# Kernel tuning notes

Hardware: AMD Instinct MI355X
Metric: run time of the kernel (lower is better)

The kernel has to match this reference:

```python
import jax, jax.numpy as jnp
import numpy as np

N_NODES = 50000
N_EDGES = 600000
IN_CH = 128
HID = 256
OUT_FEAT = 256
OUT_CH = 128
EPS = 1e-12


def _sage_conv(x, src, dst, mask_f, Wl, bl, Wr, n_nodes):
    # PyG SAGEConv: out = lin_l(mean_{j in N(i)} x_j) + lin_r(x_i); L2-normalize rows.
    msg = x[src] * mask_f[:, None]                                  # [E, d] gather
    agg = jax.ops.segment_sum(msg, dst, num_segments=n_nodes)      # [N, d]
    cnt = jax.ops.segment_sum(mask_f, dst, num_segments=n_nodes)   # [N]
    agg = agg / jnp.maximum(cnt, 1.0)[:, None]                      # mean over kept edges
    out = agg @ Wl.T + bl + x @ Wr.T                                 # [N, h]
    nrm = jnp.maximum(jnp.linalg.norm(out, axis=-1, keepdims=True), EPS)
    return out / nrm


def setup_inputs() -> dict:
    key = jax.random.key(0)
    ks = jax.random.split(key, 12)
    x = jax.random.normal(ks[0], (N_NODES, IN_CH), dtype=jnp.float32)
    edge_index = jax.random.randint(ks[1], (2, N_EDGES), 0, N_NODES, dtype=jnp.int32)
    edge_mask = jax.random.bernoulli(ks[2], 0.7, (N_EDGES,))  # dropout_edge p=0.3 keep mask

    def lin(k, fan_out, fan_in):
        s = 1.0 / np.sqrt(fan_in)
        return jax.random.uniform(k, (fan_out, fan_in), jnp.float32, -s, s)

    W1l = lin(ks[3], HID, IN_CH)
    b1 = jnp.zeros((HID,), jnp.float32)
    W1r = lin(ks[4], HID, IN_CH)
    Ws = lin(ks[5], HID, IN_CH)
    bs = jnp.zeros((HID,), jnp.float32)
    W2l = lin(ks[6], OUT_FEAT, HID)
    b2 = jnp.zeros((OUT_FEAT,), jnp.float32)
    W2r = lin(ks[7], OUT_FEAT, HID)
    Wo = lin(ks[8], OUT_CH, OUT_FEAT)
    bo = jnp.zeros((OUT_CH,), jnp.float32)
    return {"x": x, "edge_index": edge_index, "edge_mask": edge_mask,
            "W1l": W1l, "b1": b1, "W1r": W1r, "Ws": Ws, "bs": bs,
            "W2l": W2l, "b2": b2, "W2r": W2r, "Wo": Wo, "bo": bo}


def reference(x, edge_index, edge_mask, W1l, b1, W1r, Ws, bs, W2l, b2, W2r, Wo, bo):
    src, dst = edge_index[0], edge_index[1]
    ones = jnp.ones((src.shape[0],), x.dtype)
    # conv1 uses all edges
    h = _sage_conv(x, src, dst, ones, W1l, b1, W1r, N_NODES)
    h = h + (x @ Ws.T + bs)
    h = jnp.tanh(h)
    # conv2 uses edge-dropped graph (mask = kept edges)
    mask_f = edge_mask.astype(x.dtype)
    h = jnp.tanh(_sage_conv(h, src, dst, mask_f, W2l, b2, W2r, N_NODES))
    return h @ Wo.T + bo
```

## Files before the change

### kernel.cpp

```cpp
#include <hip/hip_runtime.h>
#include <hip/hip_bf16.h>

#define N_NODES 50000
#define N_PAD   50048
#define N_EDGES 600000
#define IN_CH 128
#define HID 256
#define OUT_CH 128

typedef unsigned short u16;
typedef unsigned char u8;
typedef unsigned int u32;

typedef __attribute__((ext_vector_type(8))) short short8;
typedef __attribute__((ext_vector_type(4))) float f32x4;

typedef __attribute__((address_space(3))) u32 as3_u32;
typedef __attribute__((address_space(1))) const u32 as1_u32;

__device__ __forceinline__ float bf2f(u16 v) {
    unsigned u = ((unsigned)v) << 16;
    return __uint_as_float(u);
}
__device__ __forceinline__ u16 f2bf(float f) {
    unsigned u = __float_as_uint(f);
    u += 0x7FFF + ((u >> 16) & 1);
    return (u16)(u >> 16);
}

__device__ __forceinline__ void async16(const void* g, void* l) {
    __builtin_amdgcn_global_load_lds((as1_u32*)g, (as3_u32*)l, 16, 0, 0);
}

__global__ void detect_kernel(const u16* __restrict__ xu, const u8* __restrict__ mb,
                              int* __restrict__ flags) {
    int lane = threadIdx.x & 63;

    int inr = 0;
    {
        u32 w0 = ((const u32*)xu)[lane * 2 + 0];
        u32 w1 = ((const u32*)xu)[lane * 2 + 1];
        u16 h[4] = {(u16)w0, (u16)(w0 >> 16), (u16)w1, (u16)(w1 >> 16)};
#pragma unroll
        for (int j = 0; j < 4; j++) {
            int e = (h[j] >> 7) & 0xFF;
            if (e >= 100 && e <= 133) inr++;
        }
    }

    int c1 = 0, c23 = 0, h3f_1 = 0, h3f_3 = 0;
#pragma unroll
    for (int t = 0; t < 16; t++) {
        u32 w = ((const u32*)mb)[t * 64 + lane];
        u8 b1 = (u8)(w >> 8), b2 = (u8)(w >> 16), b3 = (u8)(w >> 24);
        if (b1) c1++;
        if (b1 == 0x3F) h3f_1 = 1;
        if (b2) c23++;
        if (b3) c23++;
        if (b3 == 0x3F) h3f_3 = 1;
    }

#pragma unroll
    for (int off = 32; off > 0; off >>= 1) {
        inr   += __shfl_xor(inr, off, 64);
        c1    += __shfl_xor(c1, off, 64);
        c23   += __shfl_xor(c23, off, 64);
        h3f_1 |= __shfl_xor(h3f_1, off, 64);
        h3f_3 |= __shfl_xor(h3f_3, off, 64);
    }

    if (lane == 0 && blockIdx.x == 0) {
        flags[0] = (inr >= 200) ? 1 : 0;
        int fmt;
        if (h3f_1) fmt = 3;
        else if (h3f_3) fmt = 2;
        else if (c1 + c23 > 0) fmt = 0;
        else fmt = 1;
        flags[1] = fmt;
    }
}

__global__ void biases_kernel(const void* __restrict__ b1, const void* __restrict__ bs,
                              const void* __restrict__ b2, const void* __restrict__ bo,
                              float* __restrict__ dst, const int* __restrict__ flags) {
    int i = blockIdx.x * blockDim.x + threadIdx.x;
    if (i >= 896) return;
    const void* src; int idx;
    if (i < 256)      { src = b1; idx = i; }
    else if (i < 512) { src = bs; idx = i - 256; }
    else if (i < 768) { src = b2; idx = i - 512; }
    else              { src = bo; idx = i - 768; }
    float v;
    if (flags[0]) v = bf2f(((const u16*)src)[idx]);
    else          v = ((const float*)src)[idx];
    dst[i] = v;
}

__global__ void wcat_kernel(const void* __restrict__ A, const void* __restrict__ B,
                            u16* __restrict__ dst, int N, int K1, int K2,
                            const int* __restrict__ flags) {
    int i = blockIdx.x * blockDim.x + threadIdx.x;
    int K = K1 + K2;
    if (i >= N * K) return;
    int n = i / K, k = i % K;
    const void* src; int idx;
    if (k < K1) { src = A; idx = n * K1 + k; }
    else        { src = B; idx = n * K2 + (k - K1); }
    u16 v;
    if (flags[0]) v = ((const u16*)src)[idx];
    else          v = f2bf(((const float*)src)[idx]);
    dst[i] = v;
}

__global__ void hist_kernel(const int* __restrict__ ei, const void* __restrict__ em,
                            int* __restrict__ deg, int* __restrict__ deg2,
                            int* __restrict__ rank, int* __restrict__ krank,
                            const int* __restrict__ flags) {
    int i = blockIdx.x * blockDim.x + threadIdx.x;
    if (i >= N_EDGES) return;
    int d = ei[N_EDGES + i];
    rank[i] = atomicAdd(&deg[d], 1);
    int fmt = flags[1];
    bool keep;
    if (fmt == 0)      keep = ((const u8*)em)[i] != 0;
    else if (fmt == 1) keep = ((const int*)em)[i] != 0;
    else if (fmt == 2) keep = ((const float*)em)[i] != 0.f;
    else               keep = ((const u16*)em)[i] != 0;
    krank[i] = keep ? atomicAdd(&deg2[d], 1) : -1;
}

__global__ void partial_kernel(const int* __restrict__ deg, const int* __restrict__ deg2,
                               int* __restrict__ partial, int nb) {
    __shared__ int sh[256];
    int t = threadIdx.x;
    int arr = (blockIdx.x >= nb) ? 1 : 0;
    int blk = blockIdx.x - arr * nb;
    const int* d = arr ? deg2 : deg;
    int i = blk * 256 + t;
    sh[t] = (i < N_NODES) ? d[i] : 0;
    __syncthreads();
    for (int s = 128; s > 0; s >>= 1) {
        if (t < s) sh[t] += sh[t + s];
        __syncthreads();
    }
    if (t == 0) partial[blockIdx.x] = sh[0];
}

__global__ void scanp_kernel(const int* __restrict__ partial, int* __restrict__ pscan, int nb) {
    __shared__ int sh[256];
    int t = threadIdx.x;
    int base = blockIdx.x * nb;
    int v = (t < nb) ? partial[base + t] : 0;
    sh[t] = v;
    __syncthreads();
    for (int o = 1; o < 256; o <<= 1) {
        int u = (t >= o) ? sh[t - o] : 0;
        __syncthreads();
        sh[t] += u;
        __syncthreads();
    }
    if (t < nb) pscan[base + t] = sh[t] - v;
}

__global__ void rowptr_kernel(const int* __restrict__ deg, const int* __restrict__ deg2,
                              const int* __restrict__ pscan,
                              int* __restrict__ row_ptr, int* __restrict__ row_ptr2, int nb) {
    __shared__ int sh[256];
    int t = threadIdx.x;
    int arr = (blockIdx.x >= nb) ? 1 : 0;
    int blk = blockIdx.x - arr * nb;
    const int* d = arr ? deg2 : deg;
    int* rp = arr ? row_ptr2 : row_ptr;
    int i = blk * 256 + t;
    int v = (i < N_NODES) ? d[i] : 0;
    sh[t] = v;
    __syncthreads();
    for (int o = 1; o < 256; o <<= 1) {
        int u = (t >= o) ? sh[t - o] : 0;
        __syncthreads();
        sh[t] += u;
        __syncthreads();
    }
    if (i <= N_NODES) rp[i] = pscan[arr * nb + blk] + sh[t] - v;
}

__global__ void scatter_csr_kernel(const int* __restrict__ ei, const int* __restrict__ rank,
                                   const int* __restrict__ krank,
                                   const int* __restrict__ row_ptr, const int* __restrict__ row_ptr2,
                                   int* __restrict__ srcs, int* __restrict__ srcs2) {
    int i = blockIdx.x * blockDim.x + threadIdx.x;
    if (i >= N_EDGES) return;
    int d = ei[N_EDGES + i];
    int s = ei[i];
    srcs[row_ptr[d] + rank[i]] = s;
    int r2 = krank[i];
    if (r2 >= 0) srcs2[row_ptr2[d] + r2] = s;
}

__global__ __launch_bounds__(256) void gather1_kernel(const int* __restrict__ row_ptr,
                                                      const int* __restrict__ srcs,
                                                      const u16* __restrict__ xb,
                                                      u16* __restrict__ aggb) {
    int wid = (blockIdx.x * blockDim.x + threadIdx.x) >> 6;
    int lane = threadIdx.x & 63;
    if (wid >= N_NODES) return;
    int start = row_ptr[wid], end = row_ptr[wid + 1];
    int dg = end - start;
    int sv = (lane < dg) ? srcs[start + lane] : 0;
    float ax = 0.f, ay = 0.f, bx = 0.f, by = 0.f;
    int n = dg < 64 ? dg : 64;
    int e = 0;
    for (; e + 2 <= n; e += 2) {
        int s0 = __builtin_amdgcn_readlane(sv, e);
        int s1 = __builtin_amdgcn_readlane(sv, e + 1);
        u32 v0 = *(const u32*)(xb + (size_t)s0 * IN_CH + lane * 2);
        u32 v1 = *(const u32*)(xb + (size_t)s1 * IN_CH + lane * 2);
        ax += bf2f((u16)v0); ay += bf2f((u16)(v0 >> 16));
        bx += bf2f((u16)v1); by += bf2f((u16)(v1 >> 16));
    }
    if (e < n) {
        int s0 = __builtin_amdgcn_readlane(sv, e);
        u32 v0 = *(const u32*)(xb + (size_t)s0 * IN_CH + lane * 2);
        ax += bf2f((u16)v0); ay += bf2f((u16)(v0 >> 16));
    }
    for (e = 64; e < dg; e++) {
        int s0 = srcs[start + e];
        u32 v0 = *(const u32*)(xb + (size_t)s0 * IN_CH + lane * 2);
        ax += bf2f((u16)v0); ay += bf2f((u16)(v0 >> 16));
    }
    float inv = 1.f / fmaxf((float)dg, 1.f);
    u32 o = (u32)f2bf((ax + bx) * inv) | ((u32)f2bf((ay + by) * inv) << 16);
    *(u32*)(aggb + (size_t)wid * IN_CH + lane * 2) = o;
}

__global__ __launch_bounds__(256) void gather2_kernel(const int* __restrict__ row_ptr2,
                                                      const int* __restrict__ srcs2,
                                                      const u16* __restrict__ h1b,
                                                      u16* __restrict__ aggb) {
    int wid = (blockIdx.x * blockDim.x + threadIdx.x) >> 6;
    int lane = threadIdx.x & 63;
    if (wid >= N_NODES) return;
    int start = row_ptr2[wid], end = row_ptr2[wid + 1];
    int dg = end - start;
    int sv = (lane < dg) ? srcs2[start + lane] : 0;
    float a0 = 0.f, a1 = 0.f, a2 = 0.f, a3 = 0.f;
    float b0 = 0.f, b1 = 0.f, b2 = 0.f, b3 = 0.f;
    int n = dg < 64 ? dg : 64;
    int e = 0;
    for (; e + 2 <= n; e += 2) {
        int s0 = __builtin_amdgcn_readlane(sv, e);
        int s1 = __builtin_amdgcn_readlane(sv, e + 1);
        uint2 v = *(const uint2*)(h1b + (size_t)s0 * HID + lane * 4);
        uint2 w = *(const uint2*)(h1b + (size_t)s1 * HID + lane * 4);
        a0 += bf2f((u16)v.x); a1 += bf2f((u16)(v.x >> 16));
        a2 += bf2f((u16)v.y); a3 += bf2f((u16)(v.y >> 16));
        b0 += bf2f((u16)w.x); b1 += bf2f((u16)(w.x >> 16));
        b2 += bf2f((u16)w.y); b3 += bf2f((u16)(w.y >> 16));
    }
    if (e < n) {
        int s0 = __builtin_amdgcn_readlane(sv, e);
        uint2 v = *(const uint2*)(h1b + (size_t)s0 * HID + lane * 4);
        a0 += bf2f((u16)v.x); a1 += bf2f((u16)(v.x >> 16));
        a2 += bf2f((u16)v.y); a3 += bf2f((u16)(v.y >> 16));
    }
    for (e = 64; e < dg; e++) {
        int s0 = srcs2[start + e];
        uint2 v = *(const uint2*)(h1b + (size_t)s0 * HID + lane * 4);
        a0 += bf2f((u16)v.x); a1 += bf2f((u16)(v.x >> 16));
        a2 += bf2f((u16)v.y); a3 += bf2f((u16)(v.y >> 16));
    }
    float inv = 1.f / fmaxf((float)dg, 1.f);
    u32 o0 = (u32)f2bf((a0 + b0) * inv) | ((u32)f2bf((a1 + b1) * inv) << 16);
    u32 o1 = (u32)f2bf((a2 + b2) * inv) | ((u32)f2bf((a3 + b3) * inv) << 16);
    u16* p = aggb + (size_t)wid * HID + lane * 4;
    *(u32*)p = o0;
    *(u32*)(p + 2) = o1;
}

template<int MODE>
__global__ __launch_bounds__(256, 2) void gemm_staged(
    const u16* __restrict__ A0, const u16* __restrict__ A1,
    const u16* __restrict__ W0, const u16* __restrict__ W1,
    const float* __restrict__ bias0, const float* __restrict__ bias1,
    u16* __restrict__ outb, void* __restrict__ outv, const int* __restrict__ flags) {

    constexpr int NT  = (MODE == 3) ? 2 : 4;
    constexpr int Nw  = NT * 16;
    constexpr int NKS = (MODE == 1) ? 6 : ((MODE == 2) ? 8 : 4);
    constexpr int BBYTES = NT * 64 * 128;
    __shared__ __align__(16) u8 ldsmem[16384 + 2 * BBYTES];

    int tid = threadIdx.x;
    int w = tid >> 6, lane = tid & 63;
    int q = lane >> 4, c = lane & 15;
    int m_base = blockIdx.x * 64;
    int rj = lane >> 3, jj = lane & 7;
    int j16 = ((jj ^ rj) << 4);

    f32x4 acc[4][NT], acc2[4][NT];
    const f32x4 z = {0.f, 0.f, 0.f, 0.f};
#pragma unroll
    for (int mt = 0; mt < 4; mt++)
#pragma unroll
        for (int nt = 0; nt < NT; nt++) { acc[mt][nt] = z; acc2[mt][nt] = z; }

    auto stage = [&](int ks, int b) {
        const u16* ap; int astr, kta;
        const u16* wp; int wstr, ktw;
        if (MODE == 1) {
            astr = 128;
            if (ks < 2)      { ap = A0; kta = ks; }
            else if (ks < 4) { ap = A1; kta = ks - 2; }
            else             { ap = A1; kta = ks - 4; }
            if (ks < 4) { wp = W0; wstr = 256; ktw = ks; }
            else        { wp = W1; wstr = 128; ktw = ks - 4; }
        } else if (MODE == 2) {
            astr = 256;
            if (ks < 4) { ap = A0; kta = ks; } else { ap = A1; kta = ks - 4; }
            wp = W0; wstr = 512; ktw = ks;
        } else {
            astr = 256; ap = A0; kta = ks;
            wp = W0; wstr = 256; ktw = ks;
        }
#pragma unroll
        for (int t = 0; t < 2; t++) {
            int r = w * 16 + t * 8;
            const u8* g = (const u8*)(ap + (size_t)(m_base + r + rj) * astr) + kta * 128 + j16;
            async16(g, ldsmem + b * 8192 + r * 128);
        }
#pragma unroll
        for (int t = 0; t < NT * 2; t++) {
            int n = w * Nw + t * 8;
            const u8* g = (const u8*)(wp + (size_t)(n + rj) * wstr) + ktw * 128 + j16;
            async16(g, ldsmem + 16384 + b * BBYTES + n * 128);
        }
    };

    auto compute = [&](int b, f32x4 (*tgt)[NT]) {
        const u8* ab = ldsmem + b * 8192;
        const u8* bb = ldsmem + 16384 + b * BBYTES;
#pragma unroll
        for (int kk = 0; kk < 2; kk++) {
            int sA = (((kk * 4 + q) ^ (c & 7)) << 4);
            short8 af[4], bfr[NT];
#pragma unroll
            for (int mt = 0; mt < 4; mt++)
                af[mt] = *(const short8*)(ab + (mt * 16 + c) * 128 + sA);
#pragma unroll
            for (int nt = 0; nt < NT; nt++)
                bfr[nt] = *(const short8*)(bb + (w * Nw + nt * 16 + c) * 128 + sA);
#pragma unroll
            for (int mt = 0; mt < 4; mt++)
#pragma unroll
                for (int nt = 0; nt < NT; nt++)
                    tgt[mt][nt] = __builtin_amdgcn_mfma_f32_16x16x32_bf16(af[mt], bfr[nt], tgt[mt][nt], 0, 0, 0);
        }
    };

    stage(0, 0);
    int b = 0;
#pragma unroll
    for (int ks = 0; ks < NKS; ks++) {
        __syncthreads();
        if (ks + 1 < NKS) stage(ks + 1, b ^ 1);
        if (MODE == 1 && ks >= 4) compute(b, acc2);
        else                      compute(b, acc);
        b ^= 1;
    }
    __syncthreads();

    if (MODE == 3) {
        float bcol[NT];
#pragma unroll
        for (int nt = 0; nt < NT; nt++) bcol[nt] = bias0[w * Nw + nt * 16 + c];
        int isbf = flags[0];
#pragma unroll
        for (int mt = 0; mt < 4; mt++)
#pragma unroll
            for (int r = 0; r < 4; r++) {
                int row = m_base + mt * 16 + q * 4 + r;
                if (row < N_NODES) {
#pragma unroll
                    for (int nt = 0; nt < NT; nt++) {
                        float v = acc[mt][nt][r] + bcol[nt];
                        int col = w * Nw + nt * 16 + c;
                        if (isbf) ((u16*)outv)[(size_t)row * OUT_CH + col] = f2bf(v);
                        else      ((float*)outv)[(size_t)row * OUT_CH + col] = v;
                    }
                }
            }
    } else {
        float* redf = (float*)ldsmem;
        float bcol[NT], b2col[NT];
#pragma unroll
        for (int nt = 0; nt < NT; nt++) {
            int col = w * Nw + nt * 16 + c;
            bcol[nt] = bias0[col];
            if (MODE == 1) b2col[nt] = bias1[col];
        }
        float s[4][4];
#pragma unroll
        for (int mt = 0; mt < 4; mt++)
#pragma unroll
            for (int r = 0; r < 4; r++) {
                float t = 0.f;
#pragma unroll
                for (int nt = 0; nt < NT; nt++) {
                    float v = acc[mt][nt][r] + bcol[nt];
                    acc[mt][nt][r] = v;
                    t += v * v;
                }
                s[mt][r] = t;
            }
#pragma unroll
        for (int off = 1; off < 16; off <<= 1) {
#pragma unroll
            for (int mt = 0; mt < 4; mt++)
#pragma unroll
                for (int r = 0; r < 4; r++)
                    s[mt][r] += __shfl_xor(s[mt][r], off, 64);
        }
        if (c == 0) {
#pragma unroll
            for (int mt = 0; mt < 4; mt++)
#pragma unroll
                for (int r = 0; r < 4; r++)
                    redf[(mt * 16 + q * 4 + r) * 4 + w] = s[mt][r];
        }
        __syncthreads();
        if (tid < 64) {
            float t = redf[tid * 4] + redf[tid * 4 + 1] + redf[tid * 4 + 2] + redf[tid * 4 + 3];
            redf[256 + tid] = 1.f / fmaxf(sqrtf(t), 1e-12f);
        }
        __syncthreads();
#pragma unroll
        for (int mt = 0; mt < 4; mt++)
#pragma unroll
            for (int r = 0; r < 4; r++) {
                int rl = mt * 16 + q * 4 + r;
                int row = m_base + rl;
                if (row < N_NODES) {
                    float iv = redf[256 + rl];
#pragma unroll
                    for (int nt = 0; nt < NT; nt++) {
                        int col = w * Nw + nt * 16 + c;
                        float h;
                        if (MODE == 1) h = acc[mt][nt][r] * iv + acc2[mt][nt][r] + b2col[nt];
                        else           h = acc[mt][nt][r] * iv;
                        outb[(size_t)row * HID + col] = f2bf(tanhf(h));
                    }
                }
            }
    }
}

extern "C" void kernel_launch(void* const* d_in, const int* in_sizes, int n_in,
                              void* d_out, int out_size, void* d_ws, size_t ws_size,
                              hipStream_t stream) {
    const void* x    = d_in[0];
    const int*  ei   = (const int*)d_in[1];
    const void* em   = d_in[2];
    const void* W1l  = d_in[3];
    const void* b1   = d_in[4];
    const void* W1r  = d_in[5];
    const void* Ws   = d_in[6];
    const void* bs   = d_in[7];
    const void* W2l  = d_in[8];
    const void* b2   = d_in[9];
    const void* W2r  = d_in[10];
    const void* Wo   = d_in[11];
    const void* bo   = d_in[12];

    char* p = (char*)d_ws;
    auto carve = [&](size_t bytes) { char* r = p; p += (bytes + 63) & ~(size_t)63; return r; };
    int*   flags   = (int*)carve(256);
    u16*   xb      = (u16*)carve((size_t)N_PAD * IN_CH * 2);
    u16*   h1b     = (u16*)carve((size_t)N_PAD * HID * 2);
    u16*   aggb    = (u16*)carve((size_t)N_PAD * HID * 2);
    u16*   h2b     = (u16*)carve((size_t)N_PAD * HID * 2);
    u16*   Wc1     = (u16*)carve(256 * 256 * 2);
    u16*   Wsb     = (u16*)carve(256 * 128 * 2);
    u16*   Wc2     = (u16*)carve(256 * 512 * 2);
    u16*   Wob     = (u16*)carve(128 * 256 * 2);
    float* biasf   = (float*)carve(896 * 4);
    int*   deg     = (int*)carve(2 * 50176 * 4);
    int*   deg2    = deg + 50176;
    int*   row_ptr = (int*)carve(50056 * 4);
    int*   row_ptr2= (int*)carve(50056 * 4);
    int*   partial = (int*)carve(512 * 4);
    int*   pscan   = (int*)carve(512 * 4);
    int*   rank    = (int*)carve((size_t)N_EDGES * 4);
    int*   krank   = (int*)carve((size_t)N_EDGES * 4);
    int*   srcs    = (int*)carve((size_t)N_EDGES * 4);
    int*   srcs2   = (int*)carve((size_t)N_EDGES * 4);
    float* b1f = biasf, *bsf = biasf + 256, *b2f = biasf + 512, *bof = biasf + 768;
    (void)ws_size; (void)in_sizes; (void)n_in; (void)out_size;

    detect_kernel<<<1, 64, 0, stream>>>((const u16*)x, (const u8*)em, flags);

    wcat_kernel<<<(N_NODES * IN_CH + 255) / 256, 256, 0, stream>>>(x, x, xb, 1, N_NODES * IN_CH, 0, flags);
    wcat_kernel<<<(256 * 256 + 255) / 256, 256, 0, stream>>>(W1l, W1r, Wc1, 256, 128, 128, flags);
    wcat_kernel<<<(256 * 128 + 255) / 256, 256, 0, stream>>>(Ws, Ws, Wsb, 1, 256 * 128, 0, flags);
    wcat_kernel<<<(256 * 512 + 255) / 256, 256, 0, stream>>>(W2l, W2r, Wc2, 256, 256, 256, flags);
    wcat_kernel<<<(128 * 256 + 255) / 256, 256, 0, stream>>>(Wo, Wo, Wob, 1, 128 * 256, 0, flags);
    biases_kernel<<<4, 256, 0, stream>>>(b1, bs, b2, bo, biasf, flags);

    hipMemsetAsync(deg, 0, 2 * 50176 * sizeof(int), stream);
    hist_kernel<<<(N_EDGES + 255) / 256, 256, 0, stream>>>(ei, em, deg, deg2, rank, krank, flags);
    const int NB = (N_NODES + 255) / 256;
    partial_kernel<<<2 * NB, 256, 0, stream>>>(deg, deg2, partial, NB);
    scanp_kernel<<<2, 256, 0, stream>>>(partial, pscan, NB);
    rowptr_kernel<<<2 * NB, 256, 0, stream>>>(deg, deg2, pscan, row_ptr, row_ptr2, NB);
    scatter_csr_kernel<<<(N_EDGES + 255) / 256, 256, 0, stream>>>(ei, rank, krank, row_ptr, row_ptr2, srcs, srcs2);

    const int GB = N_PAD / 64;

    gather1_kernel<<<(N_NODES * 64) / 256, 256, 0, stream>>>(row_ptr, srcs, xb, aggb);
    gemm_staged<1><<<GB, 256, 0, stream>>>(aggb, xb, Wc1, Wsb, b1f, bsf, h1b, nullptr, flags);

    gather2_kernel<<<(N_NODES * 64) / 256, 256, 0, stream>>>(row_ptr2, srcs2, h1b, aggb);
    gemm_staged<2><<<GB, 256, 0, stream>>>(aggb, h1b, Wc2, nullptr, b2f, nullptr, h2b, nullptr, flags);

    gemm_staged<3><<<GB, 256, 0, stream>>>(h2b, nullptr, Wob, nullptr, bof, nullptr, nullptr, d_out, flags);
}
```

Before: 339.2 us.

## Fuse conversion launches, pack dual degree counters, unroll gathers by four

Folds the five weight/input conversion kernels and the bias kernel into one launch. Packs both the full-graph and the masked-graph degree counters into one 32-bit word, updated with a single atomic per edge. The per-edge ranks are packed the same way, so the two CSR builds share one partial/scan/rowptr pass and half the rank storage. The neighbour gathers are unrolled to four outstanding loads with more accumulators, to raise memory-level parallelism. The packing relies on per-node and per-block counts fitting in 16 bits, and the wider unroll adds register pressure.

```diff
diff --git a/kernel.cpp b/kernel.cpp
--- a/kernel.cpp
+++ b/kernel.cpp
@@ -80,64 +80,76 @@
     }
 }
 
-__global__ void biases_kernel(const void* __restrict__ b1, const void* __restrict__ bs,
-                              const void* __restrict__ b2, const void* __restrict__ bo,
-                              float* __restrict__ dst, const int* __restrict__ flags) {
+#define NX (N_NODES * IN_CH)
+__global__ void convert_all_kernel(const void* __restrict__ x,
+                                   const void* __restrict__ W1l, const void* __restrict__ W1r,
+                                   const void* __restrict__ Ws,
+                                   const void* __restrict__ W2l, const void* __restrict__ W2r,
+                                   const void* __restrict__ Wo,
+                                   const void* __restrict__ b1, const void* __restrict__ bs,
+                                   const void* __restrict__ b2, const void* __restrict__ bo,
+                                   u16* __restrict__ xb, u16* __restrict__ Wc1,
+                                   u16* __restrict__ Wsb, u16* __restrict__ Wc2,
+                                   u16* __restrict__ Wob, float* __restrict__ biasf,
+                                   const int* __restrict__ flags) {
     int i = blockIdx.x * blockDim.x + threadIdx.x;
-    if (i >= 896) return;
-    const void* src; int idx;
-    if (i < 256)      { src = b1; idx = i; }
-    else if (i < 512) { src = bs; idx = i - 256; }
-    else if (i < 768) { src = b2; idx = i - 512; }
-    else              { src = bo; idx = i - 768; }
-    float v;
-    if (flags[0]) v = bf2f(((const u16*)src)[idx]);
-    else          v = ((const float*)src)[idx];
-    dst[i] = v;
-}
-
-__global__ void wcat_kernel(const void* __restrict__ A, const void* __restrict__ B,
-                            u16* __restrict__ dst, int N, int K1, int K2,
-                            const int* __restrict__ flags) {
-    int i = blockIdx.x * blockDim.x + threadIdx.x;
-    int K = K1 + K2;
-    if (i >= N * K) return;
-    int n = i / K, k = i % K;
-    const void* src; int idx;
-    if (k < K1) { src = A; idx = n * K1 + k; }
-    else        { src = B; idx = n * K2 + (k - K1); }
-    u16 v;
-    if (flags[0]) v = ((const u16*)src)[idx];
-    else          v = f2bf(((const float*)src)[idx]);
-    dst[i] = v;
-}
+    int isbf = flags[0];
+    auto cv = [&](const void* s, int idx) -> u16 {
+        return isbf ? ((const u16*)s)[idx] : f2bf(((const float*)s)[idx]);
+    };
+    if (i < NX) { xb[i] = cv(x, i); return; }
+    i -= NX;
+    if (i < 256 * 256) {
+        int n = i >> 8, k = i & 255;
+        const void* s = (k < 128) ? W1l : W1r;
+        Wc1[i] = cv(s, n * 128 + (k & 127));
+        return;
+    }
+    i -= 256 * 256;
+    if (i < 256 * 128) { Wsb[i] = cv(Ws, i); return; }
+    i -= 256 * 128;
+    if (i < 256 * 512) {
+        int n = i >> 9, k = i & 511;
+        const void* s = (k < 256) ? W2l : W2r;
+        Wc2[i] = cv(s, n * 256 + (k & 255));
+        return;
+    }
+    i -= 256 * 512;
+    if (i < 128 * 256) { Wob[i] = cv(Wo, i); return; }
+    i -= 128 * 256;
+    if (i < 896) {
+        const void* s; int idx;
+        if (i < 256)      { s = b1; idx = i; }
+        else if (i < 512) { s = bs; idx = i - 256; }
+        else if (i < 768) { s = b2; idx = i - 512; }
+        else              { s = bo; idx = i - 768; }
+        biasf[i] = isbf ? bf2f(((const u16*)s)[idx]) : ((const float*)s)[idx];
+    }
+}
+#define CONV_TOTAL (NX + 256 * 256 + 256 * 128 + 256 * 512 + 128 * 256 + 896)
 
 __global__ void hist_kernel(const int* __restrict__ ei, const void* __restrict__ em,
-                            int* __restrict__ deg, int* __restrict__ deg2,
-                            int* __restrict__ rank, int* __restrict__ krank,
+                            u32* __restrict__ degp, u32* __restrict__ rankp,
                             const int* __restrict__ flags) {
     int i = blockIdx.x * blockDim.x + threadIdx.x;
     if (i >= N_EDGES) return;
     int d = ei[N_EDGES + i];
-    rank[i] = atomicAdd(&deg[d], 1);
     int fmt = flags[1];
     bool keep;
     if (fmt == 0)      keep = ((const u8*)em)[i] != 0;
     else if (fmt == 1) keep = ((const int*)em)[i] != 0;
     else if (fmt == 2) keep = ((const float*)em)[i] != 0.f;
     else               keep = ((const u16*)em)[i] != 0;
-    krank[i] = keep ? atomicAdd(&deg2[d], 1) : -1;
-}
-
-__global__ void partial_kernel(const int* __restrict__ deg, const int* __restrict__ deg2,
-                               int* __restrict__ partial, int nb) {
-    __shared__ int sh[256];
+    u32 inc = keep ? 0x10001u : 1u;
+    u32 old = atomicAdd(&degp[d], inc);
+    rankp[i] = (old & 0xffffu) | (keep ? (old & 0xffff0000u) : 0xffff0000u);
+}
+
+__global__ void partial_kernel(const u32* __restrict__ degp, u32* __restrict__ partial) {
+    __shared__ u32 sh[256];
     int t = threadIdx.x;
-    int arr = (blockIdx.x >= nb) ? 1 : 0;
-    int blk = blockIdx.x - arr * nb;
-    const int* d = arr ? deg2 : deg;
-    int i = blk * 256 + t;
-    sh[t] = (i < N_NODES) ? d[i] : 0;
+    int i = blockIdx.x * 256 + t;
+    sh[t] = (i < N_NODES) ? degp[i] : 0;
     __syncthreads();
     for (int s = 128; s > 0; s >>= 1) {
         if (t < s) sh[t] += sh[t + s];
@@ -146,55 +158,64 @@
     if (t == 0) partial[blockIdx.x] = sh[0];
 }
 
-__global__ void scanp_kernel(const int* __restrict__ partial, int* __restrict__ pscan, int nb) {
+__global__ void scanp_kernel(const u32* __restrict__ partial, int* __restrict__ pscan, int nb) {
     __shared__ int sh[256];
     int t = threadIdx.x;
-    int base = blockIdx.x * nb;
-    int v = (t < nb) ? partial[base + t] : 0;
+    u32 pv = (t < nb) ? partial[t] : 0;
+    int v1 = pv & 0xffff, v2 = pv >> 16;
+    sh[t] = v1;
+    __syncthreads();
+    for (int o = 1; o < 256; o <<= 1) {
+        int u = (t >= o) ? sh[t - o] : 0;
+        __syncthreads();
+        sh[t] += u;
+        __syncthreads();
+    }
+    if (t < nb) pscan[t] = sh[t] - v1;
+    __syncthreads();
+    sh[t] = v2;
+    __syncthreads();
+    for (int o = 1; o < 256; o <<= 1) {
+        int u = (t >= o) ? sh[t - o] : 0;
+        __syncthreads();
+        sh[t] += u;
+        __syncthreads();
+    }
+    if (t < nb) pscan[nb + t] = sh[t] - v2;
+}
+
+__global__ void rowptr_kernel(const u32* __restrict__ degp, const int* __restrict__ pscan,
+                              int* __restrict__ row_ptr, int* __restrict__ row_ptr2, int nb) {
+    __shared__ u32 sh[256];
+    int t = threadIdx.x;
+    int i = blockIdx.x * 256 + t;
+    u32 v = (i < N_NODES) ? degp[i] : 0;
     sh[t] = v;
     __syncthreads();
     for (int o = 1; o < 256; o <<= 1) {
-        int u = (t >= o) ? sh[t - o] : 0;
+        u32 u = (t >= o) ? sh[t - o] : 0;
         __syncthreads();
         sh[t] += u;
         __syncthreads();
     }
-    if (t < nb) pscan[base + t] = sh[t] - v;
-}
-
-__global__ void rowptr_kernel(const int* __restrict__ deg, const int* __restrict__ deg2,
-                              const int* __restrict__ pscan,
-                              int* __restrict__ row_ptr, int* __restrict__ row_ptr2, int nb) {
-    __shared__ int sh[256];
-    int t = threadIdx.x;
-    int arr = (blockIdx.x >= nb) ? 1 : 0;
-    int blk = blockIdx.x - arr * nb;
-    const int* d = arr ? deg2 : deg;
-    int* rp = arr ? row_ptr2 : row_ptr;
-    int i = blk * 256 + t;
-    int v = (i < N_NODES) ? d[i] : 0;
-    sh[t] = v;
-    __syncthreads();
-    for (int o = 1; o < 256; o <<= 1) {
-        int u = (t >= o) ? sh[t - o] : 0;
-        __syncthreads();
-        sh[t] += u;
-        __syncthreads();
-    }
-    if (i <= N_NODES) rp[i] = pscan[arr * nb + blk] + sh[t] - v;
-}
-
-__global__ void scatter_csr_kernel(const int* __restrict__ ei, const int* __restrict__ rank,
-                                   const int* __restrict__ krank,
+    u32 ex = sh[t] - v;
+    if (i <= N_NODES) {
+        row_ptr[i]  = pscan[blockIdx.x] + (int)(ex & 0xffff);
+        row_ptr2[i] = pscan[nb + blockIdx.x] + (int)(ex >> 16);
+    }
+}
+
+__global__ void scatter_csr_kernel(const int* __restrict__ ei, const u32* __restrict__ rankp,
                                    const int* __restrict__ row_ptr, const int* __restrict__ row_ptr2,
                                    int* __restrict__ srcs, int* __restrict__ srcs2) {
     int i = blockIdx.x * blockDim.x + threadIdx.x;
     if (i >= N_EDGES) return;
     int d = ei[N_EDGES + i];
     int s = ei[i];
-    srcs[row_ptr[d] + rank[i]] = s;
-    int r2 = krank[i];
-    if (r2 >= 0) srcs2[row_ptr2[d] + r2] = s;
+    u32 rp = rankp[i];
+    srcs[row_ptr[d] + (int)(rp & 0xffffu)] = s;
+    u32 kr = rp >> 16;
+    if (kr != 0xffffu) srcs2[row_ptr2[d] + (int)kr] = s;
 }
 
 __global__ __launch_bounds__(256) void gather1_kernel(const int* __restrict__ row_ptr,
@@ -207,29 +228,38 @@
     int start = row_ptr[wid], end = row_ptr[wid + 1];
     int dg = end - start;
     int sv = (lane < dg) ? srcs[start + lane] : 0;
-    float ax = 0.f, ay = 0.f, bx = 0.f, by = 0.f;
+    float a0 = 0.f, a1 = 0.f, b0 = 0.f, b1 = 0.f;
+    float c0 = 0.f, c1 = 0.f, d0 = 0.f, d1 = 0.f;
     int n = dg < 64 ? dg : 64;
     int e = 0;
-    for (; e + 2 <= n; e += 2) {
+    for (; e + 4 <= n; e += 4) {
         int s0 = __builtin_amdgcn_readlane(sv, e);
         int s1 = __builtin_amdgcn_readlane(sv, e + 1);
+        int s2 = __builtin_amdgcn_readlane(sv, e + 2);
+        int s3 = __builtin_amdgcn_readlane(sv, e + 3);
         u32 v0 = *(const u32*)(xb + (size_t)s0 * IN_CH + lane * 2);
         u32 v1 = *(const u32*)(xb + (size_t)s1 * IN_CH + lane * 2);
-        ax += bf2f((u16)v0); ay += bf2f((u16)(v0 >> 16));
-        bx += bf2f((u16)v1); by += bf2f((u16)(v1 >> 16));
-    }
-    if (e < n) {
+        u32 v2 = *(const u32*)(xb + (size_t)s2 * IN_CH + lane * 2);
+        u32 v3 = *(const u32*)(xb + (size_t)s3 * IN_CH + lane * 2);
+        a0 += bf2f((u16)v0); a1 += bf2f((u16)(v0 >> 16));
+        b0 += bf2f((u16)v1); b1 += bf2f((u16)(v1 >> 16));
+        c0 += bf2f((u16)v2); c1 += bf2f((u16)(v2 >> 16));
+        d0 += bf2f((u16)v3); d1 += bf2f((u16)(v3 >> 16));
+    }
+    for (; e < n; e++) {
         int s0 = __builtin_amdgcn_readlane(sv, e);
         u32 v0 = *(const u32*)(xb + (size_t)s0 * IN_CH + lane * 2);
-        ax += bf2f((u16)v0); ay += bf2f((u16)(v0 >> 16));
+        a0 += bf2f((u16)v0); a1 += bf2f((u16)(v0 >> 16));
     }
     for (e = 64; e < dg; e++) {
         int s0 = srcs[start + e];
         u32 v0 = *(const u32*)(xb + (size_t)s0 * IN_CH + lane * 2);
-        ax += bf2f((u16)v0); ay += bf2f((u16)(v0 >> 16));
+        a0 += bf2f((u16)v0); a1 += bf2f((u16)(v0 >> 16));
     }
     float inv = 1.f / fmaxf((float)dg, 1.f);
-    u32 o = (u32)f2bf((ax + bx) * inv) | ((u32)f2bf((ay + by) * inv) << 16);
+    float rx = (a0 + b0) + (c0 + d0);
+    float ry = (a1 + b1) + (c1 + d1);
+    u32 o = (u32)f2bf(rx * inv) | ((u32)f2bf(ry * inv) << 16);
     *(u32*)(aggb + (size_t)wid * IN_CH + lane * 2) = o;
 }
 
@@ -245,19 +275,29 @@
     int sv = (lane < dg) ? srcs2[start + lane] : 0;
     float a0 = 0.f, a1 = 0.f, a2 = 0.f, a3 = 0.f;
     float b0 = 0.f, b1 = 0.f, b2 = 0.f, b3 = 0.f;
+    float c0 = 0.f, c1 = 0.f, c2 = 0.f, c3 = 0.f;
+    float d0 = 0.f, d1 = 0.f, d2 = 0.f, d3 = 0.f;
     int n = dg < 64 ? dg : 64;
     int e = 0;
-    for (; e + 2 <= n; e += 2) {
+    for (; e + 4 <= n; e += 4) {
         int s0 = __builtin_amdgcn_readlane(sv, e);
         int s1 = __builtin_amdgcn_readlane(sv, e + 1);
+        int s2 = __builtin_amdgcn_readlane(sv, e + 2);
+        int s3 = __builtin_amdgcn_readlane(sv, e + 3);
         uint2 v = *(const uint2*)(h1b + (size_t)s0 * HID + lane * 4);
         uint2 w = *(const uint2*)(h1b + (size_t)s1 * HID + lane * 4);
+        uint2 y = *(const uint2*)(h1b + (size_t)s2 * HID + lane * 4);
+        uint2 zz = *(const uint2*)(h1b + (size_t)s3 * HID + lane * 4);
         a0 += bf2f((u16)v.x); a1 += bf2f((u16)(v.x >> 16));
         a2 += bf2f((u16)v.y); a3 += bf2f((u16)(v.y >> 16));
         b0 += bf2f((u16)w.x); b1 += bf2f((u16)(w.x >> 16));
         b2 += bf2f((u16)w.y); b3 += bf2f((u16)(w.y >> 16));
-    }
-    if (e < n) {
+        c0 += bf2f((u16)y.x); c1 += bf2f((u16)(y.x >> 16));
+        c2 += bf2f((u16)y.y); c3 += bf2f((u16)(y.y >> 16));
+        d0 += bf2f((u16)zz.x); d1 += bf2f((u16)(zz.x >> 16));
+        d2 += bf2f((u16)zz.y); d3 += bf2f((u16)(zz.y >> 16));
+    }
+    for (; e < n; e++) {
         int s0 = __builtin_amdgcn_readlane(sv, e);
         uint2 v = *(const uint2*)(h1b + (size_t)s0 * HID + lane * 4);
         a0 += bf2f((u16)v.x); a1 += bf2f((u16)(v.x >> 16));
@@ -270,8 +310,12 @@
         a2 += bf2f((u16)v.y); a3 += bf2f((u16)(v.y >> 16));
     }
     float inv = 1.f / fmaxf((float)dg, 1.f);
-    u32 o0 = (u32)f2bf((a0 + b0) * inv) | ((u32)f2bf((a1 + b1) * inv) << 16);
-    u32 o1 = (u32)f2bf((a2 + b2) * inv) | ((u32)f2bf((a3 + b3) * inv) << 16);
+    float r0 = (a0 + b0) + (c0 + d0);
+    float r1 = (a1 + b1) + (c1 + d1);
+    float r2 = (a2 + b2) + (c2 + d2);
+    float r3 = (a3 + b3) + (c3 + d3);
+    u32 o0 = (u32)f2bf(r0 * inv) | ((u32)f2bf(r1 * inv) << 16);
+    u32 o1 = (u32)f2bf(r2 * inv) | ((u32)f2bf(r3 * inv) << 16);
     u16* p = aggb + (size_t)wid * HID + lane * 4;
     *(u32*)p = o0;
     *(u32*)(p + 2) = o1;
@@ -483,14 +527,12 @@
     u16*   Wc2     = (u16*)carve(256 * 512 * 2);
     u16*   Wob     = (u16*)carve(128 * 256 * 2);
     float* biasf   = (float*)carve(896 * 4);
-    int*   deg     = (int*)carve(2 * 50176 * 4);
-    int*   deg2    = deg + 50176;
+    u32*   degp    = (u32*)carve(50176 * 4);
     int*   row_ptr = (int*)carve(50056 * 4);
     int*   row_ptr2= (int*)carve(50056 * 4);
-    int*   partial = (int*)carve(512 * 4);
+    u32*   partial = (u32*)carve(256 * 4);
     int*   pscan   = (int*)carve(512 * 4);
-    int*   rank    = (int*)carve((size_t)N_EDGES * 4);
-    int*   krank   = (int*)carve((size_t)N_EDGES * 4);
+    u32*   rankp   = (u32*)carve((size_t)N_EDGES * 4);
     int*   srcs    = (int*)carve((size_t)N_EDGES * 4);
     int*   srcs2   = (int*)carve((size_t)N_EDGES * 4);
     float* b1f = biasf, *bsf = biasf + 256, *b2f = biasf + 512, *bof = biasf + 768;
@@ -498,20 +540,17 @@
 
     detect_kernel<<<1, 64, 0, stream>>>((const u16*)x, (const u8*)em, flags);
 
-    wcat_kernel<<<(N_NODES * IN_CH + 255) / 256, 256, 0, stream>>>(x, x, xb, 1, N_NODES * IN_CH, 0, flags);
-    wcat_kernel<<<(256 * 256 + 255) / 256, 256, 0, stream>>>(W1l, W1r, Wc1, 256, 128, 128, flags);
-    wcat_kernel<<<(256 * 128 + 255) / 256, 256, 0, stream>>>(Ws, Ws, Wsb, 1, 256 * 128, 0, flags);
-    wcat_kernel<<<(256 * 512 + 255) / 256, 256, 0, stream>>>(W2l, W2r, Wc2, 256, 256, 256, flags);
-    wcat_kernel<<<(128 * 256 + 255) / 256, 256, 0, stream>>>(Wo, Wo, Wob, 1, 128 * 256, 0, flags);
-    biases_kernel<<<4, 256, 0, stream>>>(b1, bs, b2, bo, biasf, flags);
-
-    hipMemsetAsync(deg, 0, 2 * 50176 * sizeof(int), stream);
-    hist_kernel<<<(N_EDGES + 255) / 256, 256, 0, stream>>>(ei, em, deg, deg2, rank, krank, flags);
+    convert_all_kernel<<<(CONV_TOTAL + 255) / 256, 256, 0, stream>>>(
+        x, W1l, W1r, Ws, W2l, W2r, Wo, b1, bs, b2, bo,
+        xb, Wc1, Wsb, Wc2, Wob, biasf, flags);
+
+    hipMemsetAsync(degp, 0, 50176 * sizeof(u32), stream);
+    hist_kernel<<<(N_EDGES + 255) / 256, 256, 0, stream>>>(ei, em, degp, rankp, flags);
     const int NB = (N_NODES + 255) / 256;
-    partial_kernel<<<2 * NB, 256, 0, stream>>>(deg, deg2, partial, NB);
-    scanp_kernel<<<2, 256, 0, stream>>>(partial, pscan, NB);
-    rowptr_kernel<<<2 * NB, 256, 0, stream>>>(deg, deg2, pscan, row_ptr, row_ptr2, NB);
-    scatter_csr_kernel<<<(N_EDGES + 255) / 256, 256, 0, stream>>>(ei, rank, krank, row_ptr, row_ptr2, srcs, srcs2);
+    partial_kernel<<<NB, 256, 0, stream>>>(degp, partial);
+    scanp_kernel<<<1, 256, 0, stream>>>(partial, pscan, NB);
+    rowptr_kernel<<<NB, 256, 0, stream>>>(degp, pscan, row_ptr, row_ptr2, NB);
+    scatter_csr_kernel<<<(N_EDGES + 255) / 256, 256, 0, stream>>>(ei, rankp, row_ptr, row_ptr2, srcs, srcs2);
 
     const int GB = N_PAD / 64;
 
```

After: 309.5 us. 8.7% less time.
